# Performance work log

Hardware: AMD Instinct MI355X
Metric: run time of the kernel (lower is better)

The kernel has to match this reference:

```python
import jax, jax.numpy as jnp
import numpy as np

B, N, D, H = 2, 2048, 1024, 16
DH = D // H  # 64


def setup_inputs() -> dict:
    key = jax.random.key(0)
    k1, k2, k3, k4, k5 = jax.random.split(key, 5)
    x = jax.random.normal(k1, (B, N, D), dtype=jnp.float32)
    # per-head kqv Linear weights, stacked: [H, D, 3*DH] (acts as x @ W)
    W_kqv = jax.random.normal(k2, (H, D, 3 * DH), dtype=jnp.float32) * 0.02
    b_kqv = jax.random.normal(k3, (H, 3 * DH), dtype=jnp.float32) * 0.02
    W_proj = jax.random.normal(k4, (D, D), dtype=jnp.float32) * 0.02
    b_proj = jax.random.normal(k5, (D,), dtype=jnp.float32) * 0.02
    return {"x": x, "W_kqv": W_kqv, "b_kqv": b_kqv, "W_proj": W_proj, "b_proj": b_proj}


def reference(x, W_kqv, b_kqv, W_proj, b_proj):
    # per-head projections, all heads batched: [B, H, N, 3*DH]
    kqv = jnp.einsum('bnd,hde->bhne', x, W_kqv) + b_kqv[None, :, None, :]
    # original chunk order is k, q, v
    k, q, v = jnp.split(kqv, 3, axis=-1)  # each [B, H, N, DH]
    # scores: A = q @ k^T / sqrt(DH)  -> [B, H, N, N]
    A = jnp.einsum('bhnd,bhmd->bhnm', q, k) / jnp.sqrt(jnp.asarray(DH, x.dtype))
    causal = jnp.tril(jnp.ones((N, N), dtype=bool))
    A = jnp.where(causal[None, None, :, :], A, -jnp.inf)
    attn = jax.nn.softmax(A, axis=-1)
    sa = jnp.einsum('bhnm,bhmd->bhnd', attn, v)          # [B, H, N, DH]
    sa = sa.transpose(0, 2, 1, 3).reshape(B, N, D)        # concat heads
    out = sa @ W_proj.T + b_proj                          # output projection
    return out
```

## Files before the change

### kernel.cpp

```cpp
#include <hip/hip_runtime.h>
#include <hip/hip_bf16.h>
#include <cstdint>
#include <cstddef>

#define B_  2
#define N_  2048
#define D_  1024
#define H_  16
#define DH_ 64
#define E3_ 192

typedef __attribute__((ext_vector_type(8))) short short8;
typedef __attribute__((ext_vector_type(8))) unsigned short ushort8v;
typedef __attribute__((ext_vector_type(4))) float floatx4;

static __device__ __forceinline__ unsigned short f2bf(float f) {
  union { float f; unsigned u; } c; c.f = f;
  unsigned r = c.u + 0x7fffu + ((c.u >> 16) & 1u);
  return (unsigned short)(r >> 16);
}

#define MFMA(a,b,c) __builtin_amdgcn_mfma_f32_16x16x32_bf16((a),(b),(c),0,0,0)

#define GL_LDS16(g, l) __builtin_amdgcn_global_load_lds( \
    (const __attribute__((address_space(1))) void*)(g),  \
    (__attribute__((address_space(3))) void*)(l), 16, 0, 0)

__global__ __launch_bounds__(256) void k_prep(const float* __restrict__ x,
                                              const float* __restrict__ Wkqv,
                                              const float* __restrict__ Wproj,
                                              unsigned short* __restrict__ Xb,
                                              unsigned short* __restrict__ Wt,
                                              unsigned short* __restrict__ Wpb) {
  __shared__ float tile[64][65];
  int bx = blockIdx.x, t = threadIdx.x;
  if (bx < 2048 || bx >= 2816) {
    const float* in = (bx < 2048) ? x : Wproj;
    unsigned short* out = (bx < 2048) ? Xb : Wpb;
    int i = ((bx < 2048) ? bx : bx - 2816) * 256 + t;
    const float4* p = (const float4*)in + (size_t)i * 2;
    float4 a = p[0], b = p[1];
    ushort8v o;
    o[0]=f2bf(a.x); o[1]=f2bf(a.y); o[2]=f2bf(a.z); o[3]=f2bf(a.w);
    o[4]=f2bf(b.x); o[5]=f2bf(b.y); o[6]=f2bf(b.z); o[7]=f2bf(b.w);
    *((ushort8v*)out + i) = o;
    return;
  }
  int idx = bx - 2048;
  int d0 = (idx & 15) * 64, rem = idx >> 4;
  int cat = rem % 3, h = rem / 3, e0 = cat * 64;
  const float* Wp = Wkqv + (size_t)h * D_ * E3_;
  int dr = t >> 2, ec = (t & 3) * 16;
#pragma unroll
  for (int j = 0; j < 16; j += 4) {
    float4 wv = *(const float4*)&Wp[(size_t)(d0 + dr) * E3_ + e0 + ec + j];
    tile[dr][ec + j + 0] = wv.x; tile[dr][ec + j + 1] = wv.y;
    tile[dr][ec + j + 2] = wv.z; tile[dr][ec + j + 3] = wv.w;
  }
  __syncthreads();
  int er = t >> 2, dc = (t & 3) * 16;
  ushort8v o0, o1;
#pragma unroll
  for (int j = 0; j < 8; j++) o0[j] = f2bf(tile[dc + j][er]);
#pragma unroll
  for (int j = 0; j < 8; j++) o1[j] = f2bf(tile[dc + 8 + j][er]);
  size_t o = ((size_t)(cat * 1024 + h * 64 + er)) * D_ + d0 + dc;
  *(ushort8v*)&Wt[o]     = o0;
  *(ushort8v*)&Wt[o + 8] = o1;
}

__global__ __launch_bounds__(256, 2) void k_qkv(const unsigned short* __restrict__ Xb,
                                                const unsigned short* __restrict__ Wt,
                                                const float* __restrict__ bkqv,
                                                unsigned short* __restrict__ Qb,
                                                unsigned short* __restrict__ Kb,
                                                unsigned short* __restrict__ Vt) {
  __shared__ unsigned short LDSq[32768];
  const int t = threadIdx.x;
  const int wid = t >> 6, lane = t & 63, quad = lane >> 4, l16 = lane & 15;
  const int wm = (wid >> 1) * 64, wn = (wid & 1) * 64;
  const int m0 = blockIdx.x * 128, c0 = blockIdx.y * 128;

  floatx4 acc[4][4];
#pragma unroll
  for (int i = 0; i < 4; i++)
#pragma unroll
    for (int j = 0; j < 4; j++) acc[i][j] = (floatx4){0.f, 0.f, 0.f, 0.f};

  const int slr = t >> 3;
  const int sco = ((t & 7) ^ (slr & 7)) * 8;
  const unsigned short* gA0 = Xb + (size_t)(m0 +  0 + slr) * D_ + sco;
  const unsigned short* gA1 = Xb + (size_t)(m0 + 32 + slr) * D_ + sco;
  const unsigned short* gA2 = Xb + (size_t)(m0 + 64 + slr) * D_ + sco;
  const unsigned short* gA3 = Xb + (size_t)(m0 + 96 + slr) * D_ + sco;
  const unsigned short* gB0 = Wt + (size_t)(c0 +  0 + slr) * D_ + sco;
  const unsigned short* gB1 = Wt + (size_t)(c0 + 32 + slr) * D_ + sco;
  const unsigned short* gB2 = Wt + (size_t)(c0 + 64 + slr) * D_ + sco;
  const unsigned short* gB3 = Wt + (size_t)(c0 + 96 + slr) * D_ + sco;
#define SA(qq, s, bb) GL_LDS16(gA##qq + (s) * 64, &LDSq[(bb) * 8192 + (qq) * 2048 + t * 8])
#define SB(qq, s, bb) GL_LDS16(gB##qq + (s) * 64, &LDSq[16384 + (bb) * 8192 + (qq) * 2048 + t * 8])
#define STAGE(s, bb) do { SA(0,s,bb); SA(1,s,bb); SA(2,s,bb); SA(3,s,bb); \
                          SB(0,s,bb); SB(1,s,bb); SB(2,s,bb); SB(3,s,bb); } while (0)

  const int aoff0 = ((quad)     ^ (l16 & 7)) * 8;
  const int aoff1 = ((4 + quad) ^ (l16 & 7)) * 8;

  STAGE(0, 0);
  STAGE(1, 1);

  for (int i = 0; i < 16; i++) {
    const int buf = i & 1;
    const int soA = buf * 8192, soB = 16384 + buf * 8192;
    if (i + 1 < 16) { asm volatile("s_waitcnt vmcnt(8)" ::: "memory"); }
    else            { asm volatile("s_waitcnt vmcnt(0)" ::: "memory"); }
    __builtin_amdgcn_s_barrier();
    __builtin_amdgcn_sched_barrier(0);
    short8 a[4][2], b[4][2];
#pragma unroll
    for (int mi = 0; mi < 4; mi++) {
      a[mi][0] = *(const short8*)&LDSq[soA + (wm + mi * 16 + l16) * 64 + aoff0];
      a[mi][1] = *(const short8*)&LDSq[soA + (wm + mi * 16 + l16) * 64 + aoff1];
    }
#pragma unroll
    for (int ni = 0; ni < 4; ni++) {
      b[ni][0] = *(const short8*)&LDSq[soB + (wn + ni * 16 + l16) * 64 + aoff0];
      b[ni][1] = *(const short8*)&LDSq[soB + (wn + ni * 16 + l16) * 64 + aoff1];
    }
    __builtin_amdgcn_s_setprio(1);
#pragma unroll
    for (int mi = 0; mi < 4; mi++)
#pragma unroll
      for (int ni = 0; ni < 4; ni++) {
        acc[mi][ni] = MFMA(a[mi][0], b[ni][0], acc[mi][ni]);
        acc[mi][ni] = MFMA(a[mi][1], b[ni][1], acc[mi][ni]);
      }
    __builtin_amdgcn_s_setprio(0);
    __builtin_amdgcn_s_barrier();
    __builtin_amdgcn_sched_barrier(0);
    if (i + 2 < 16) STAGE(i + 2, buf);
  }
#undef SA
#undef SB
#undef STAGE

  __syncthreads();
  unsigned short* scr = &LDSq[wid * 4096];
  const int cat = c0 >> 10;
  const int h   = ((c0 + wn) >> 6) & 15;
  const int bb  = (m0 + wm) >> 11;
  const int n0b = (m0 + wm) & (N_ - 1);
  const int l8 = lane & 7, lh = lane >> 3;
  if (cat < 2) {
    const float scale = (cat == 1) ? 0.18033688011112042f : 1.0f;
    float bias[4];
#pragma unroll
    for (int ni = 0; ni < 4; ni++) bias[ni] = bkqv[h * E3_ + cat * 64 + ni * 16 + l16];
#pragma unroll
    for (int mi = 0; mi < 4; mi++)
#pragma unroll
      for (int ni = 0; ni < 4; ni++)
#pragma unroll
        for (int r = 0; r < 4; r++) {
          int rl = mi * 16 + quad * 4 + r, cl = ni * 16 + l16;
          scr[rl * 64 + (((cl >> 3) ^ (rl & 7)) * 8) + (cl & 7)] =
              f2bf((acc[mi][ni][r] + bias[ni]) * scale);
        }
    asm volatile("s_waitcnt lgkmcnt(0)" ::: "memory");
    unsigned short* dst = (cat == 0) ? Kb : Qb;
#pragma unroll
    for (int j = 0; j < 8; j++) {
      int rl = j * 8 + lh;
      short8 vv = *(const short8*)&scr[rl * 64 + ((l8 ^ lh) * 8)];
      *(short8*)&dst[((size_t)(bb * H_ + h) * N_ + n0b + rl) * DH_ + l8 * 8] = vv;
    }
  } else {
    float bias[4];
#pragma unroll
    for (int ni = 0; ni < 4; ni++) bias[ni] = bkqv[h * E3_ + 128 + ni * 16 + l16];
#pragma unroll
    for (int mi = 0; mi < 4; mi++)
#pragma unroll
      for (int ni = 0; ni < 4; ni++)
#pragma unroll
        for (int r = 0; r < 4; r++) {
          int nl = mi * 16 + quad * 4 + r, e = ni * 16 + l16;
          scr[e * 64 + (((nl >> 3) ^ (e & 7)) * 8) + (nl & 7)] =
              f2bf(acc[mi][ni][r] + bias[ni]);
        }
    asm volatile("s_waitcnt lgkmcnt(0)" ::: "memory");
#pragma unroll
    for (int j = 0; j < 8; j++) {
      int le = j * 8 + lh;
      short8 vv = *(const short8*)&scr[le * 64 + ((l8 ^ lh) * 8)];
      *(short8*)&Vt[((size_t)(bb * H_ + h) * DH_ + le) * N_ + n0b + l8 * 8] = vv;
    }
  }
}

__global__ __launch_bounds__(256) void k_flash(const unsigned short* __restrict__ Qb,
                                               const unsigned short* __restrict__ Kb,
                                               const unsigned short* __restrict__ Vt,
                                               unsigned short* __restrict__ sab) {
  int bh = blockIdx.x;
  int yr = blockIdx.y, g = yr >> 3, o = yr & 7;
  int qb = (g == 0) ? o : (g == 1) ? 31 - o : (g == 2) ? 8 + o : 23 - o;
  int q0b = qb * 64;
  int wave = threadIdx.x >> 6;
  int lane = threadIdx.x & 63, quad = lane >> 4, l16 = lane & 15;
  const unsigned short* Qp = Qb + (size_t)bh * N_ * DH_;
  const unsigned short* Kp = Kb + (size_t)bh * N_ * DH_;
  const unsigned short* Vp = Vt + (size_t)bh * DH_ * N_;
  __shared__ unsigned short Klds[2][2 * 64 * 32];
  __shared__ unsigned short Vlds[2][2 * 64 * 32];
  __shared__ unsigned short Plds[4][16 * 64];
  unsigned short* P = Plds[wave];

  int q0w = q0b + wave * 16;
  short8 qf0 = *(const short8*)&Qp[(q0w + l16) * DH_ + quad * 8];
  short8 qf1 = *(const short8*)&Qp[(q0w + l16) * DH_ + 32 + quad * 8];

  int swz = ((lane & 3) ^ ((lane >> 3) & 3)) * 8;
  const unsigned short* gK = Kp + (size_t)(wave * 16 + (lane >> 2)) * DH_ + swz;
  const unsigned short* gV = Vp + (size_t)(wave * 16 + (lane >> 2)) * N_ + swz;
  int lofs = (wave * 16) * 32;
  int xr = ((l16 >> 1) & 3) * 8;
  int pxr = l16 & 7;

#define FSTAGE(ii, bb) do {                                              \
    size_t ko_ = (size_t)(ii) * 64 * DH_; int vo_ = (ii) * 64;           \
    GL_LDS16(gK + ko_,      &Klds[bb][lofs]);                            \
    GL_LDS16(gK + ko_ + 32, &Klds[bb][lofs + 64 * 32]);                  \
    GL_LDS16(gV + vo_,      &Vlds[bb][lofs]);                            \
    GL_LDS16(gV + vo_ + 32, &Vlds[bb][lofs + 64 * 32]);                  \
  } while (0)

  floatx4 O[4];
  float lr = 0.f;
#pragma unroll
  for (int r = 0; r < 4; r++) O[r] = (floatx4){0.f, 0.f, 0.f, 0.f};

  int nt = (q0b >> 6) + 1;
  FSTAGE(0, 0);
  if (nt > 1) FSTAGE(1, 1);

  for (int i = 0; i < nt; i++) {
    int buf = i & 1;
    if (i + 1 < nt) { asm volatile("s_waitcnt vmcnt(4)" ::: "memory"); }
    else            { asm volatile("s_waitcnt vmcnt(0)" ::: "memory"); }
    __builtin_amdgcn_s_barrier();
    __builtin_amdgcn_sched_barrier(0);
    short8 kf[4][2], vf[4][2];
#pragma unroll
    for (int c = 0; c < 4; c++) {
      kf[c][0] = *(const short8*)&Klds[buf][(c * 16 + l16) * 32 + ((quad * 8) ^ xr)];
      kf[c][1] = *(const short8*)&Klds[buf][(64 + c * 16 + l16) * 32 + ((quad * 8) ^ xr)];
      vf[c][0] = *(const short8*)&Vlds[buf][(c * 16 + l16) * 32 + ((quad * 8) ^ xr)];
      vf[c][1] = *(const short8*)&Vlds[buf][(64 + c * 16 + l16) * 32 + ((quad * 8) ^ xr)];
    }
    floatx4 s[4];
    __builtin_amdgcn_s_setprio(1);
#pragma unroll
    for (int c = 0; c < 4; c++) {
      s[c] = (floatx4){0.f, 0.f, 0.f, 0.f};
      s[c] = MFMA(kf[c][0], qf0, s[c]);
      s[c] = MFMA(kf[c][1], qf1, s[c]);
    }
    __builtin_amdgcn_s_setprio(0);
    if (i == nt - 1) {
#pragma unroll
      for (int c = 0; c < 4; c++)
#pragma unroll
        for (int r = 0; r < 4; r++) {
          int key = c * 16 + quad * 4 + r;
          if (key > wave * 16 + l16) s[c][r] = -1e30f;
        }
    }
#pragma unroll
    for (int c = 0; c < 4; c++)
#pragma unroll
      for (int r = 0; r < 4; r++)
        s[c][r] = __builtin_amdgcn_exp2f(s[c][r]);
#pragma unroll
    for (int c = 0; c < 4; c++)
      lr += (s[c][0] + s[c][1]) + (s[c][2] + s[c][3]);
#pragma unroll
    for (int c = 0; c < 4; c++) {
      unsigned plo = (unsigned)f2bf(s[c][0]) | ((unsigned)f2bf(s[c][1]) << 16);
      unsigned phi = (unsigned)f2bf(s[c][2]) | ((unsigned)f2bf(s[c][3]) << 16);
      int ch = c * 2 + (quad >> 1);
      uint2 pk; pk.x = plo; pk.y = phi;
      *(uint2*)&P[l16 * 64 + ((ch ^ pxr) * 8) + (quad & 1) * 4] = pk;
    }
    __asm__ volatile("s_waitcnt lgkmcnt(0)" ::: "memory");
    short8 pa0 = *(const short8*)&P[l16 * 64 + ((quad ^ pxr) * 8)];
    short8 pa1 = *(const short8*)&P[l16 * 64 + (((quad + 4) ^ pxr) * 8)];
    __asm__ volatile("" ::: "memory");
    __builtin_amdgcn_s_setprio(1);
#pragma unroll
    for (int dt = 0; dt < 4; dt++) {
      O[dt] = MFMA(pa0, vf[dt][0], O[dt]);
      O[dt] = MFMA(pa1, vf[dt][1], O[dt]);
    }
    __builtin_amdgcn_s_setprio(0);
    __builtin_amdgcn_s_barrier();
    __builtin_amdgcn_sched_barrier(0);
    if (i + 2 < nt) FSTAGE(i + 2, buf);
  }
#undef FSTAGE

  lr += __shfl_xor(lr, 16);
  lr += __shfl_xor(lr, 32);

  int b = bh >> 4, h = bh & 15;
#pragma unroll
  for (int r = 0; r < 4; r++) {
    float inv = 1.0f / __shfl(lr, quad * 4 + r);
    size_t base = ((size_t)b * N_ + q0w + quad * 4 + r) * D_ + h * DH_;
#pragma unroll
    for (int dt = 0; dt < 4; dt++) sab[base + dt * 16 + l16] = f2bf(O[dt][r] * inv);
  }
}

__global__ __launch_bounds__(512) void k_proj(const unsigned short* __restrict__ sab,
                                              const unsigned short* __restrict__ Wpb,
                                              const float* __restrict__ bproj,
                                              float* __restrict__ out) {
  __shared__ unsigned short LDSp[32768];
  const int t = threadIdx.x;
  const int wid = t >> 6, lane = t & 63, quad = lane >> 4, l16 = lane & 15;
  const int wr = wid >> 1, wc = wid & 1;
  const int bid = blockIdx.x;
  const int m0 = (bid >> 3) * 128, c0 = (bid & 7) * 128;

  floatx4 acc[2][4];
#pragma unroll
  for (int i = 0; i < 2; i++)
#pragma unroll
    for (int j = 0; j < 4; j++) acc[i][j] = (floatx4){0.f, 0.f, 0.f, 0.f};

  const int slr = t >> 3;
  const int sco = ((t & 7) ^ (slr & 7)) * 8;
  const unsigned short* gA0 = sab + (size_t)(m0 +  0 + slr) * D_ + sco;
  const unsigned short* gA1 = sab + (size_t)(m0 + 64 + slr) * D_ + sco;
  const unsigned short* gB0 = Wpb + (size_t)(c0 +  0 + slr) * D_ + sco;
  const unsigned short* gB1 = Wpb + (size_t)(c0 + 64 + slr) * D_ + sco;
#define PA(gp, q, s, bb) GL_LDS16((gp) + (s) * 64, &LDSp[(bb) * 8192 + (q) * 4096 + t * 8])
#define PB(gp, q, s, bb) GL_LDS16((gp) + (s) * 64, &LDSp[16384 + (bb) * 8192 + (q) * 4096 + t * 8])

  const int aoff0 = ((quad)     ^ (l16 & 7)) * 8;
  const int aoff1 = ((4 + quad) ^ (l16 & 7)) * 8;
  const unsigned short* Abase = &LDSp[(wr * 32 + l16) * 64];
  const unsigned short* Bbase = &LDSp[16384 + (wc * 64 + l16) * 64];

  PA(gA0, 0, 0, 0); PA(gA1, 1, 0, 0); PB(gB0, 0, 0, 0); PB(gB1, 1, 0, 0);
  PA(gA0, 0, 1, 1); PA(gA1, 1, 1, 1); PB(gB0, 0, 1, 1); PB(gB1, 1, 1, 1);

  for (int i = 0; i < 16; i++) {
    const int buf = i & 1;
    const int so = buf * 8192;
    if (i + 1 < 16) { asm volatile("s_waitcnt vmcnt(4)" ::: "memory"); }
    else            { asm volatile("s_waitcnt vmcnt(0)" ::: "memory"); }
    __builtin_amdgcn_s_barrier();
    __builtin_amdgcn_sched_barrier(0);
    short8 a[2][2], b[4][2];
#pragma unroll
    for (int mi = 0; mi < 2; mi++) {
      a[mi][0] = *(const short8*)&Abase[so + mi * 1024 + aoff0];
      a[mi][1] = *(const short8*)&Abase[so + mi * 1024 + aoff1];
    }
#pragma unroll
    for (int ni = 0; ni < 4; ni++) {
      b[ni][0] = *(const short8*)&Bbase[so + ni * 1024 + aoff0];
      b[ni][1] = *(const short8*)&Bbase[so + ni * 1024 + aoff1];
    }
    __builtin_amdgcn_s_setprio(1);
#pragma unroll
    for (int mi = 0; mi < 2; mi++)
#pragma unroll
      for (int ni = 0; ni < 4; ni++) {
        acc[mi][ni] = MFMA(a[mi][0], b[ni][0], acc[mi][ni]);
        acc[mi][ni] = MFMA(a[mi][1], b[ni][1], acc[mi][ni]);
      }
    __builtin_amdgcn_s_setprio(0);
    __builtin_amdgcn_s_barrier();
    __builtin_amdgcn_sched_barrier(0);
    if (i + 2 < 16) {
      PA(gA0, 0, i + 2, buf); PA(gA1, 1, i + 2, buf);
      PB(gB0, 0, i + 2, buf); PB(gB1, 1, i + 2, buf);
    }
  }

#pragma unroll
  for (int mi = 0; mi < 2; mi++)
#pragma unroll
    for (int ni = 0; ni < 4; ni++) {
      int col = c0 + wc * 64 + ni * 16 + l16;
      int grow = m0 + wr * 32 + mi * 16 + quad * 4;
      float bias = bproj[col];
#pragma unroll
      for (int r = 0; r < 4; r++)
        out[(size_t)(grow + r) * D_ + col] = acc[mi][ni][r] + bias;
    }
#undef PA
#undef PB
}

extern "C" void kernel_launch(void* const* d_in, const int* in_sizes, int n_in,
                              void* d_out, int out_size, void* d_ws, size_t ws_size,
                              hipStream_t stream) {
  const float* x     = (const float*)d_in[0];
  const float* Wkqv  = (const float*)d_in[1];
  const float* bkqv  = (const float*)d_in[2];
  const float* Wproj = (const float*)d_in[3];
  const float* bproj = (const float*)d_in[4];
  float* out = (float*)d_out;

  char* w = (char*)d_ws;
  unsigned short* Xb  = (unsigned short*)(w);
  unsigned short* Wt  = (unsigned short*)(w + (8u  << 20));
  unsigned short* Wpb = (unsigned short*)(w + (14u << 20));
  unsigned short* Qb  = (unsigned short*)(w + (16u << 20));
  unsigned short* Kb  = (unsigned short*)(w + (24u << 20));
  unsigned short* Vt  = (unsigned short*)(w + (32u << 20));
  unsigned short* sa  = (unsigned short*)(w + (40u << 20));

  k_prep<<<2048 + 768 + 512, 256, 0, stream>>>(x, Wkqv, Wproj, Xb, Wt, Wpb);
  k_qkv<<<dim3(B_ * N_ / 128, 3072 / 128), 256, 0, stream>>>(Xb, Wt, bkqv, Qb, Kb, Vt);
  k_flash<<<dim3(B_ * H_, N_ / 64), 256, 0, stream>>>(Qb, Kb, Vt, sa);
  k_proj<<<(B_ * N_ / 128) * (D_ / 128), 512, 0, stream>>>(sa, Wpb, bproj, out);
}
```

Baseline: 168.4 us.

## Split long causal query blocks across two KV ranges with separate combine kernel

Query blocks in the second half of the sequence are split into two work items, one covering keys 0-1023 and one covering the remaining causal range. Partial unnormalised outputs and row sums go to float scratch buffers, and a new normalisation kernel adds them and writes bf16. This evens out per-block work and raises the block count from 32 to 48 per head to cut the tail imbalance. The cost is an extra kernel launch and the fp32 partial-output traffic. Merging is valid without max tracking because the kernel never subtracts a running max.

```diff
diff --git a/kernel.cpp b/kernel.cpp
--- a/kernel.cpp
+++ b/kernel.cpp
@@ -200,11 +200,20 @@
 __global__ __launch_bounds__(256) void k_flash(const unsigned short* __restrict__ Qb,
                                                const unsigned short* __restrict__ Kb,
                                                const unsigned short* __restrict__ Vt,
-                                               unsigned short* __restrict__ sab) {
+                                               unsigned short* __restrict__ sab,
+                                               float* __restrict__ Oacc,
+                                               float* __restrict__ lracc) {
   int bh = blockIdx.x;
-  int yr = blockIdx.y, g = yr >> 3, o = yr & 7;
-  int qb = (g == 0) ? o : (g == 1) ? 31 - o : (g == 2) ? 8 + o : 23 - o;
+  int yy = blockIdx.y;
+  int kind, qb;
+  if (yy < 16) { kind = 1; qb = 16 + yy; }
+  else { int i2 = (yy - 16) >> 1;
+         if (yy & 1) { kind = 2; qb = 31 - i2; }
+         else        { kind = 0; qb = 15 - i2; } }
   int q0b = qb * 64;
+  const int i0 = (kind == 2) ? 16 : 0;
+  const int i1 = (kind == 1) ? 16 : qb + 1;
+  const int ntl = i1 - i0;
   int wave = threadIdx.x >> 6;
   int lane = threadIdx.x & 63, quad = lane >> 4, l16 = lane & 15;
   const unsigned short* Qp = Qb + (size_t)bh * N_ * DH_;
@@ -239,13 +248,12 @@
 #pragma unroll
   for (int r = 0; r < 4; r++) O[r] = (floatx4){0.f, 0.f, 0.f, 0.f};
 
-  int nt = (q0b >> 6) + 1;
-  FSTAGE(0, 0);
-  if (nt > 1) FSTAGE(1, 1);
-
-  for (int i = 0; i < nt; i++) {
-    int buf = i & 1;
-    if (i + 1 < nt) { asm volatile("s_waitcnt vmcnt(4)" ::: "memory"); }
+  FSTAGE(i0, 0);
+  if (ntl > 1) FSTAGE(i0 + 1, 1);
+
+  for (int i = i0; i < i1; i++) {
+    int buf = (i - i0) & 1;
+    if (i + 1 < i1) { asm volatile("s_waitcnt vmcnt(4)" ::: "memory"); }
     else            { asm volatile("s_waitcnt vmcnt(0)" ::: "memory"); }
     __builtin_amdgcn_s_barrier();
     __builtin_amdgcn_sched_barrier(0);
@@ -266,7 +274,7 @@
       s[c] = MFMA(kf[c][1], qf1, s[c]);
     }
     __builtin_amdgcn_s_setprio(0);
-    if (i == nt - 1) {
+    if (i == i1 - 1 && kind != 1) {
 #pragma unroll
       for (int c = 0; c < 4; c++)
 #pragma unroll
@@ -304,7 +312,7 @@
     __builtin_amdgcn_s_setprio(0);
     __builtin_amdgcn_s_barrier();
     __builtin_amdgcn_sched_barrier(0);
-    if (i + 2 < nt) FSTAGE(i + 2, buf);
+    if (i + 2 < i1) FSTAGE(i + 2, buf);
   }
 #undef FSTAGE
 
@@ -312,13 +320,49 @@
   lr += __shfl_xor(lr, 32);
 
   int b = bh >> 4, h = bh & 15;
-#pragma unroll
-  for (int r = 0; r < 4; r++) {
-    float inv = 1.0f / __shfl(lr, quad * 4 + r);
-    size_t base = ((size_t)b * N_ + q0w + quad * 4 + r) * D_ + h * DH_;
-#pragma unroll
-    for (int dt = 0; dt < 4; dt++) sab[base + dt * 16 + l16] = f2bf(O[dt][r] * inv);
-  }
+  if (kind == 0) {
+#pragma unroll
+    for (int r = 0; r < 4; r++) {
+      float inv = 1.0f / __shfl(lr, quad * 4 + r);
+      size_t base = ((size_t)b * N_ + q0w + quad * 4 + r) * D_ + h * DH_;
+#pragma unroll
+      for (int dt = 0; dt < 4; dt++) sab[base + dt * 16 + l16] = f2bf(O[dt][r] * inv);
+    }
+  } else {
+    int slot = (kind == 2) ? 1 : 0;
+    float* Oa = Oacc + (size_t)slot * (32u * 1024 * 64)
+              + ((size_t)bh * 1024 + (q0w - 1024)) * 64;
+#pragma unroll
+    for (int r = 0; r < 4; r++)
+#pragma unroll
+      for (int dt = 0; dt < 4; dt++)
+        Oa[(quad * 4 + r) * 64 + dt * 16 + l16] = O[dt][r];
+    if (lane < 16)
+      lracc[(size_t)slot * (32 * 1024) + bh * 1024 + (q0w - 1024) + l16] = lr;
+  }
+}
+
+__global__ __launch_bounds__(256) void k_norm(const float* __restrict__ Oacc,
+                                              const float* __restrict__ lracc,
+                                              unsigned short* __restrict__ sab) {
+  int o8 = blockIdx.x * 256 + threadIdx.x;
+  int chunk = o8 & 127;
+  int np = (o8 >> 7) & 1023;
+  int b = o8 >> 17;
+  int h = chunk >> 3, dh0 = (chunk & 7) * 8;
+  int bh = b * 16 + h;
+  size_t obase = ((size_t)bh * 1024 + np) * 64 + dh0;
+  const float4* p0 = (const float4*)(Oacc + obase);
+  const float4* p1 = (const float4*)(Oacc + (size_t)32 * 1024 * 64 + obase);
+  float4 a0 = p0[0], a1 = p0[1], c0 = p1[0], c1 = p1[1];
+  float l = lracc[bh * 1024 + np] + lracc[32 * 1024 + bh * 1024 + np];
+  float inv = 1.0f / l;
+  ushort8v o;
+  o[0] = f2bf((a0.x + c0.x) * inv); o[1] = f2bf((a0.y + c0.y) * inv);
+  o[2] = f2bf((a0.z + c0.z) * inv); o[3] = f2bf((a0.w + c0.w) * inv);
+  o[4] = f2bf((a1.x + c1.x) * inv); o[5] = f2bf((a1.y + c1.y) * inv);
+  o[6] = f2bf((a1.z + c1.z) * inv); o[7] = f2bf((a1.w + c1.w) * inv);
+  *(ushort8v*)&sab[((size_t)b * N_ + 1024 + np) * D_ + h * 64 + dh0] = o;
 }
 
 __global__ __launch_bounds__(512) void k_proj(const unsigned short* __restrict__ sab,
@@ -423,9 +467,12 @@
   unsigned short* Kb  = (unsigned short*)(w + (24u << 20));
   unsigned short* Vt  = (unsigned short*)(w + (32u << 20));
   unsigned short* sa  = (unsigned short*)(w + (40u << 20));
+  float*          Oac = (float*)(w + (48u << 20));
+  float*          lrc = (float*)(w + (64u << 20));
 
   k_prep<<<2048 + 768 + 512, 256, 0, stream>>>(x, Wkqv, Wproj, Xb, Wt, Wpb);
   k_qkv<<<dim3(B_ * N_ / 128, 3072 / 128), 256, 0, stream>>>(Xb, Wt, bkqv, Qb, Kb, Vt);
-  k_flash<<<dim3(B_ * H_, N_ / 64), 256, 0, stream>>>(Qb, Kb, Vt, sa);
+  k_flash<<<dim3(B_ * H_, 48), 256, 0, stream>>>(Qb, Kb, Vt, sa, Oac, lrc);
+  k_norm<<<1024, 256, 0, stream>>>(Oac, lrc, sa);
   k_proj<<<(B_ * N_ / 128) * (D_ / 128), 512, 0, stream>>>(sa, Wpb, bproj, out);
 }
```

New measurement: 171.1 us. No clear change (+1.6%).
